# Kernel tuning notes

Hardware: AMD Instinct MI355X
Metric: run time of the kernel (lower is better)

The kernel has to match this reference:

```python
import jax, jax.numpy as jnp
import numpy as np

OUT_H, OUT_W = 7, 7
SPATIAL_SCALE = 1.0


def setup_inputs() -> dict:
    key = jax.random.key(0)
    B, C, H, W = 4, 256, 64, 64
    N = 128
    features = jax.random.normal(key, (B, C, H, W), dtype=jnp.float32)
    rng = np.random.default_rng(0)
    bidx = rng.integers(0, B, N)
    x1 = rng.integers(0, W - 8, N)
    y1 = rng.integers(0, H - 8, N)
    x2 = np.minimum(x1 + rng.integers(4, 48, N), W - 1)
    y2 = np.minimum(y1 + rng.integers(4, 48, N), H - 1)
    rois = jnp.asarray(np.stack([bidx, x1, y1, x2, y2], axis=1), dtype=jnp.int32)
    return {"features": features, "rois": rois}


def _bin_bounds(n_bins, bin_sz, roi_sz):
    # h_start = int(h*bin_h); h_end = int((h+1)*bin_h); then clamp as in torch code
    bins = jnp.arange(n_bins)
    start = jnp.floor(bins[None, :] * bin_sz[:, None]).astype(jnp.int32)
    end = jnp.floor((bins[None, :] + 1) * bin_sz[:, None]).astype(jnp.int32)
    start = jnp.minimum(start, roi_sz[:, None] - 1)
    end = jnp.minimum(end, roi_sz[:, None])
    return start, end  # [N, n_bins]


def _roi_pool(features, rois):
    B, C, H, W = features.shape
    b = rois[:, 0]
    coords = (rois[:, 1:5].astype(jnp.float32) * SPATIAL_SCALE).astype(jnp.int32)
    x1, y1, x2, y2 = coords[:, 0], coords[:, 1], coords[:, 2], coords[:, 3]
    roi_h = y2 - y1 + 1  # inclusive slice y1:y2+1
    roi_w = x2 - x1 + 1
    bin_h = roi_h.astype(jnp.float32) / OUT_H
    bin_w = roi_w.astype(jnp.float32) / OUT_W

    hs, he = _bin_bounds(OUT_H, bin_h, roi_h)  # [N, OUT_H]
    ws, we = _bin_bounds(OUT_W, bin_w, roi_w)  # [N, OUT_W]
    valid = (he > hs)[:, :, None] & (we > ws)[:, None, :]  # [N, OUT_H, OUT_W]

    yy = jnp.arange(H)
    xx = jnp.arange(W)
    # absolute-coordinate bin masks (factorized along H and W)
    mask_h = (yy[None, None, :] >= (y1[:, None] + hs)[:, :, None]) & (
        yy[None, None, :] < (y1[:, None] + he)[:, :, None])  # [N, OUT_H, H]
    mask_w = (xx[None, None, :] >= (x1[:, None] + ws)[:, :, None]) & (
        xx[None, None, :] < (x1[:, None] + we)[:, :, None])  # [N, OUT_W, W]

    feat = features[b]  # [N, C, H, W] gather per ROI
    NEG = jnp.array(-jnp.inf, features.dtype)
    # reduce H per output row bin (OUT_H is small, fixed)
    rows = [jnp.where(mask_h[:, i, None, :, None], feat, NEG).max(axis=2)
            for i in range(OUT_H)]  # each [N, C, W]
    rowmax = jnp.stack(rows, axis=1)  # [N, OUT_H, C, W]
    cols = [jnp.where(mask_w[:, j, None, None, :], rowmax, NEG).max(axis=3)
            for j in range(OUT_W)]  # each [N, OUT_H, C]
    pooled = jnp.stack(cols, axis=3)  # [N, OUT_H, C, OUT_W]
    pooled = jnp.transpose(pooled, (0, 2, 1, 3))  # [N, C, OUT_H, OUT_W]
    # empty bins (h_end<=h_start or w_end<=w_start) stay zero, as in the torch code
    return jnp.where(valid[:, None, :, :], pooled, jnp.zeros((), features.dtype))


def reference(features, rois):
    return _roi_pool(features, rois)
```

## Files before the change

### kernel.cpp

```cpp
#include <hip/hip_runtime.h>
#include <math.h>

#define OUT_H 7
#define OUT_W 7
#define NBINS 49
#define LDS_STRIDE 65

__global__ __launch_bounds__(256) void roipool_wave(
    const float* __restrict__ feat, const int* __restrict__ rois,
    float* __restrict__ out)
{
    constexpr int C = 256, H = 64, W = 64;
    __shared__ float racc_lds[4][OUT_H * LDS_STRIDE];

    const int bx  = blockIdx.x;
    const int n   = bx >> 6;
    const int cg  = bx & 63;

    const int tid  = threadIdx.x;
    const int lane = tid & 63;
    const int wave = tid >> 6;
    const int c    = cg * 4 + wave;

    const int* r = rois + n * 5;
    const int b  = r[0];
    const int x1 = r[1];
    const int y1 = r[2];
    const int x2 = r[3];
    const int y2 = r[4];
    const int roi_h = y2 - y1 + 1;
    const int roi_w = x2 - x1 + 1;

    const float* plane = feat + ((size_t)(b * C + c)) * (H * W);

    float racc[OUT_H];
    #pragma unroll
    for (int ph = 0; ph < OUT_H; ++ph) racc[ph] = -INFINITY;

    int y = y1;
    #pragma unroll
    for (int ph = 0; ph < OUT_H; ++ph) {
        const int yend = y1 + ((ph + 1) * roi_h) / OUT_H;
        for (; y < yend; ++y) {
            racc[ph] = fmaxf(racc[ph], plane[y * W + lane]);
        }
    }

    #pragma unroll
    for (int ph = 0; ph < OUT_H; ++ph) {
        racc_lds[wave][ph * LDS_STRIDE + lane] = racc[ph];
    }

    if (lane < NBINS) {
        const int ph = lane / OUT_W;
        const int pw = lane - ph * OUT_W;

        int hs = (ph * roi_h) / OUT_H;
        int he = ((ph + 1) * roi_h) / OUT_H;
        int ws = (pw * roi_w) / OUT_W;
        int we = ((pw + 1) * roi_w) / OUT_W;

        float result = 0.0f;
        if (he > hs && we > ws) {
            float m = -INFINITY;
            const float* seg = &racc_lds[wave][ph * LDS_STRIDE + x1];
            for (int x = ws; x < we; ++x) m = fmaxf(m, seg[x]);
            result = m;
        }
        out[((size_t)(n * C + c)) * NBINS + lane] = result;
    }
}

extern "C" void kernel_launch(void* const* d_in, const int* in_sizes, int n_in,
                              void* d_out, int out_size, void* d_ws, size_t ws_size,
                              hipStream_t stream) {
    const float* feat = (const float*)d_in[0];
    const int*   rois = (const int*)d_in[1];
    float*       out  = (float*)d_out;

    const int N = in_sizes[1] / 5;
    const int n_blocks = N * 64;

    roipool_wave<<<n_blocks, 256, 0, stream>>>(feat, rois, out);
}
```

Measured before the change: 87.52 us.

## Stage ROI rows into LDS with direct global-to-LDS DMA loads

Replaces the per-lane register row-max loop with buffer loads that go straight from global memory into LDS, 16 bytes per lane, four rows per chunk. Each output bin is then computed by one lane scanning its full 2D window in LDS. The aim is wider, fewer load instructions that skip register staging. The cost is more serial LDS work per bin lane and a much larger LDS footprint (about 50KB per block), which can lower occupancy.

```diff
diff --git a/kernel.cpp b/kernel.cpp
--- a/kernel.cpp
+++ b/kernel.cpp
@@ -4,19 +4,24 @@
 #define OUT_H 7
 #define OUT_W 7
 #define NBINS 49
-#define LDS_STRIDE 65
 
-__global__ __launch_bounds__(256) void roipool_wave(
+#define CHUNK_FLOATS 260
+#define MAX_CHUNKS 12
+#define WAVE_LDS_FLOATS (MAX_CHUNKS * CHUNK_FLOATS)
+
+typedef __attribute__((address_space(3))) void lds_void_t;
+typedef const __attribute__((address_space(1))) void gbl_void_t;
+
+__global__ __launch_bounds__(256) void roipool_dma(
     const float* __restrict__ feat, const int* __restrict__ rois,
     float* __restrict__ out)
 {
     constexpr int C = 256, H = 64, W = 64;
-    __shared__ float racc_lds[4][OUT_H * LDS_STRIDE];
+    __shared__ float lds[4 * WAVE_LDS_FLOATS];
 
-    const int bx  = blockIdx.x;
-    const int n   = bx >> 6;
-    const int cg  = bx & 63;
-
+    const int bx   = blockIdx.x;
+    const int n    = bx >> 6;
+    const int cg   = bx & 63;
     const int tid  = threadIdx.x;
     const int lane = tid & 63;
     const int wave = tid >> 6;
@@ -32,41 +37,44 @@
     const int roi_w = x2 - x1 + 1;
 
     const float* plane = feat + ((size_t)(b * C + c)) * (H * W);
+    float* wlds = &lds[wave * WAVE_LDS_FLOATS];
 
-    float racc[OUT_H];
-    #pragma unroll
-    for (int ph = 0; ph < OUT_H; ++ph) racc[ph] = -INFINITY;
+    const int l4 = lane >> 4;
+    const int lq = lane & 15;
+    const int nchunks = (roi_h + 3) >> 2;
+    for (int k = 0; k < nchunks; ++k) {
+        int y = y1 + 4 * k + l4;
+        y = y < 63 ? y : 63;
+        const float* g = plane + y * W + lq * 4;
+        __builtin_amdgcn_global_load_lds(
+            (gbl_void_t*)g, (lds_void_t*)(wlds + k * CHUNK_FLOATS), 16, 0, 0);
+    }
+    __builtin_amdgcn_s_waitcnt(0);
 
-    int y = y1;
-    #pragma unroll
-    for (int ph = 0; ph < OUT_H; ++ph) {
-        const int yend = y1 + ((ph + 1) * roi_h) / OUT_H;
-        for (; y < yend; ++y) {
-            racc[ph] = fmaxf(racc[ph], plane[y * W + lane]);
+    const int ph = lane / OUT_W;
+    const int pw = lane - ph * OUT_W;
+
+    int hs = (ph * roi_h) / OUT_H;
+    int he = ((ph + 1) * roi_h) / OUT_H;
+    hs = hs < roi_h - 1 ? hs : roi_h - 1;
+    he = he < roi_h ? he : roi_h;
+    int ws = (pw * roi_w) / OUT_W;
+    int we = ((pw + 1) * roi_w) / OUT_W;
+    ws = ws < roi_w - 1 ? ws : roi_w - 1;
+    we = we < roi_w ? we : roi_w;
+
+    float result = 0.0f;
+    if (lane < NBINS && he > hs && we > ws) {
+        float m = -INFINITY;
+        for (int dy = hs; dy < he; ++dy) {
+            const float* rowp = &wlds[(dy >> 2) * CHUNK_FLOATS + (dy & 3) * W + x1];
+            for (int x = ws; x < we; ++x) {
+                m = fmaxf(m, rowp[x]);
+            }
         }
+        result = m;
     }
-
-    #pragma unroll
-    for (int ph = 0; ph < OUT_H; ++ph) {
-        racc_lds[wave][ph * LDS_STRIDE + lane] = racc[ph];
-    }
-
     if (lane < NBINS) {
-        const int ph = lane / OUT_W;
-        const int pw = lane - ph * OUT_W;
-
-        int hs = (ph * roi_h) / OUT_H;
-        int he = ((ph + 1) * roi_h) / OUT_H;
-        int ws = (pw * roi_w) / OUT_W;
-        int we = ((pw + 1) * roi_w) / OUT_W;
-
-        float result = 0.0f;
-        if (he > hs && we > ws) {
-            float m = -INFINITY;
-            const float* seg = &racc_lds[wave][ph * LDS_STRIDE + x1];
-            for (int x = ws; x < we; ++x) m = fmaxf(m, seg[x]);
-            result = m;
-        }
         out[((size_t)(n * C + c)) * NBINS + lane] = result;
     }
 }
@@ -81,5 +89,5 @@
     const int N = in_sizes[1] / 5;
     const int n_blocks = N * 64;
 
-    roipool_wave<<<n_blocks, 256, 0, stream>>>(feat, rois, out);
+    roipool_dma<<<n_blocks, 256, 0, stream>>>(feat, rois, out);
 }
```

Result: no change. 87.28 us (-0.3%).

## Use fixed-count clamped loads per bin and one-wave blocks per channel

Applied to the files above, without the earlier changes.

Replaces the variable-length per-row max loop with a fixed four-row batch of independent, clamped loads per output row bin. A second batch of four runs only when roi_h exceeds 28. The column reduction becomes a fixed eight-wide clamped gather from LDS. Launches one 64-thread block per (ROI, channel) instead of four waves per block. The aim is more loads in flight and less latency-bound serial looping, at the cost of redundant duplicate loads for small bins and more registers.

```diff
diff --git a/kernel.cpp b/kernel.cpp
--- a/kernel.cpp
+++ b/kernel.cpp
@@ -4,70 +4,100 @@
 #define OUT_H 7
 #define OUT_W 7
 #define NBINS 49
-#define LDS_STRIDE 65
 
-__global__ __launch_bounds__(256) void roipool_wave(
+__global__ __launch_bounds__(64) void roipool_v9(
     const float* __restrict__ feat, const int* __restrict__ rois,
     float* __restrict__ out)
 {
     constexpr int C = 256, H = 64, W = 64;
-    __shared__ float racc_lds[4][OUT_H * LDS_STRIDE];
+    __shared__ float racc_lds[OUT_H][W + 1];
 
-    const int bx  = blockIdx.x;
-    const int n   = bx >> 6;
-    const int cg  = bx & 63;
-
-    const int tid  = threadIdx.x;
-    const int lane = tid & 63;
-    const int wave = tid >> 6;
-    const int c    = cg * 4 + wave;
+    const int bx   = blockIdx.x;
+    const int n    = bx >> 8;
+    const int c    = bx & 255;
+    const int lane = threadIdx.x;
 
     const int* r = rois + n * 5;
     const int b  = r[0];
     const int x1 = r[1];
     const int y1 = r[2];
-    const int x2 = r[3];
-    const int y2 = r[4];
-    const int roi_h = y2 - y1 + 1;
-    const int roi_w = x2 - x1 + 1;
+    const int roi_w = r[3] - x1 + 1;
+    const int roi_h = r[4] - y1 + 1;
 
     const float* plane = feat + ((size_t)(b * C + c)) * (H * W);
 
+    int hb[OUT_H + 1];
+#pragma unroll
+    for (int k = 0; k <= OUT_H; ++k) hb[k] = (k * roi_h) / OUT_H;
+
     float racc[OUT_H];
-    #pragma unroll
-    for (int ph = 0; ph < OUT_H; ++ph) racc[ph] = -INFINITY;
-
-    int y = y1;
-    #pragma unroll
-    for (int ph = 0; ph < OUT_H; ++ph) {
-        const int yend = y1 + ((ph + 1) * roi_h) / OUT_H;
-        for (; y < yend; ++y) {
-            racc[ph] = fmaxf(racc[ph], plane[y * W + lane]);
+    {
+        float v[OUT_H][4];
+#pragma unroll
+        for (int ph = 0; ph < OUT_H; ++ph) {
+            const int yb = y1 + hb[ph];
+            int yl = y1 + hb[ph + 1] - 1;
+            yl = yl > yb ? yl : yb;
+#pragma unroll
+            for (int j = 0; j < 4; ++j) {
+                int y = yb + j;
+                y = y < yl ? y : yl;
+                v[ph][j] = plane[y * W + lane];
+            }
         }
+#pragma unroll
+        for (int ph = 0; ph < OUT_H; ++ph)
+            racc[ph] = fmaxf(fmaxf(v[ph][0], v[ph][1]),
+                             fmaxf(v[ph][2], v[ph][3]));
+    }
+    if (roi_h > 28) {
+        float v[OUT_H][4];
+#pragma unroll
+        for (int ph = 0; ph < OUT_H; ++ph) {
+            const int yb = y1 + hb[ph];
+            const int yl = y1 + hb[ph + 1] - 1;
+#pragma unroll
+            for (int j = 0; j < 4; ++j) {
+                int y = yb + 4 + j;
+                y = y < yl ? y : yl;
+                v[ph][j] = plane[y * W + lane];
+            }
+        }
+#pragma unroll
+        for (int ph = 0; ph < OUT_H; ++ph)
+            racc[ph] = fmaxf(racc[ph],
+                             fmaxf(fmaxf(v[ph][0], v[ph][1]),
+                                   fmaxf(v[ph][2], v[ph][3])));
     }
 
-    #pragma unroll
-    for (int ph = 0; ph < OUT_H; ++ph) {
-        racc_lds[wave][ph * LDS_STRIDE + lane] = racc[ph];
-    }
+#pragma unroll
+    for (int ph = 0; ph < OUT_H; ++ph) racc_lds[ph][lane] = racc[ph];
 
     if (lane < NBINS) {
         const int ph = lane / OUT_W;
         const int pw = lane - ph * OUT_W;
 
-        int hs = (ph * roi_h) / OUT_H;
-        int he = ((ph + 1) * roi_h) / OUT_H;
-        int ws = (pw * roi_w) / OUT_W;
-        int we = ((pw + 1) * roi_w) / OUT_W;
+        const int hsL = (ph * roi_h) / OUT_H;
+        const int heL = ((ph + 1) * roi_h) / OUT_H;
+        const int ws  = (pw * roi_w) / OUT_W;
+        const int we  = ((pw + 1) * roi_w) / OUT_W;
 
-        float result = 0.0f;
-        if (he > hs && we > ws) {
-            float m = -INFINITY;
-            const float* seg = &racc_lds[wave][ph * LDS_STRIDE + x1];
-            for (int x = ws; x < we; ++x) m = fmaxf(m, seg[x]);
-            result = m;
+        const int xs = x1 + ws;
+        int xl = x1 + we - 1;
+        xl = xl > xs ? xl : xs;
+
+        float g[8];
+#pragma unroll
+        for (int j = 0; j < 8; ++j) {
+            int x = xs + j;
+            x = x < xl ? x : xl;
+            g[j] = racc_lds[ph][x];
         }
-        out[((size_t)(n * C + c)) * NBINS + lane] = result;
+        float m = fmaxf(fmaxf(fmaxf(g[0], g[1]), fmaxf(g[2], g[3])),
+                        fmaxf(fmaxf(g[4], g[5]), fmaxf(g[6], g[7])));
+
+        const bool valid = (heL > hsL) && (we > ws);
+        out[((size_t)(n * C + c)) * NBINS + lane] = valid ? m : 0.0f;
     }
 }
 
@@ -79,7 +109,7 @@
     float*       out  = (float*)d_out;
 
     const int N = in_sizes[1] / 5;
-    const int n_blocks = N * 64;
+    const int n_blocks = N * 256;
 
-    roipool_wave<<<n_blocks, 256, 0, stream>>>(feat, rois, out);
+    roipool_v9<<<n_blocks, 64, 0, stream>>>(feat, rois, out);
 }
```

After: 77.75 us. 11.2% less time.
